# Kernel tuning notes

Measured on AMD Instinct MI355X. Metric: run time of the kernel, lower is better.

The kernel has to match this reference:

```python
import jax, jax.numpy as jnp
import numpy as np

DIM = 512
WIN = 7
HEADS = 16
N = WIN * WIN            # 49 tokens per window
NW = 64                  # windows per image (56/7)^2
BATCH = 32               # images
B_ = BATCH * NW          # 2048 window-batches
TABLE = (2 * WIN - 1) ** 2  # 169


def _relative_position_index(win):
    # Faithful to the TF construction in __init__.
    coords = np.stack(np.meshgrid(np.arange(win), np.arange(win), indexing='ij'))
    coords = coords.reshape(2, -1).T                      # [N, 2]
    rel = coords[:, None, :] - coords[None, :, :]          # [N, N, 2]
    rel = rel + (win - 1)
    idx = rel[..., 0] * (2 * win - 1) + rel[..., 1]        # [N, N]
    return jnp.asarray(idx, dtype=jnp.int32)


def setup_inputs() -> dict:
    key = jax.random.key(0)
    ks = jax.random.split(key, 7)
    x = jax.random.normal(ks[0], (B_, N, DIM), dtype=jnp.float32)
    # shifted-window additive mask: 0 where allowed, -100 where blocked
    mask = jnp.where(jax.random.uniform(ks[1], (NW, N, N)) < 0.8, 0.0, -100.0).astype(jnp.float32)
    qkv_w = jax.random.normal(ks[2], (DIM, 3 * DIM), dtype=jnp.float32) * 0.02
    qkv_b = jax.random.normal(ks[3], (3 * DIM,), dtype=jnp.float32) * 0.02
    proj_w = jax.random.normal(ks[4], (DIM, DIM), dtype=jnp.float32) * 0.02
    proj_b = jax.random.normal(ks[5], (DIM,), dtype=jnp.float32) * 0.02
    rel_table = jax.random.normal(ks[6], (TABLE, HEADS), dtype=jnp.float32) * 0.02
    rel_index = _relative_position_index(WIN)
    return {"x": x, "mask": mask, "qkv_w": qkv_w, "qkv_b": qkv_b,
            "proj_w": proj_w, "proj_b": proj_b,
            "rel_table": rel_table, "rel_index": rel_index}


def reference(x, mask, qkv_w, qkv_b, proj_w, proj_b, rel_table, rel_index):
    B, n, C = x.shape
    hd = C // HEADS
    scale = hd ** (-0.5)
    # qkv projection -> [3, B, H, N, hd]
    qkv = (x @ qkv_w + qkv_b).reshape(B, n, 3, HEADS, hd).transpose(2, 0, 3, 1, 4)
    q, k, v = qkv[0] * scale, qkv[1], qkv[2]
    attn = jnp.einsum('bhnd,bhmd->bhnm', q, k)             # [B, H, N, N]
    # relative position bias gather: [N*N] -> [N, N, H] -> [H, N, N]
    bias = rel_table[rel_index.reshape(-1)].reshape(n, n, HEADS).transpose(2, 0, 1)
    attn = attn + bias[None]
    nW = mask.shape[0]
    attn = attn.reshape(B // nW, nW, HEADS, n, n) + mask[None, :, None]
    attn = attn.reshape(-1, HEADS, n, n)
    attn = jax.nn.softmax(attn, axis=-1)
    out = jnp.einsum('bhnm,bhmd->bhnd', attn, v)           # [B, H, N, hd]
    out = out.transpose(0, 2, 1, 3).reshape(B, n, C)
    return out @ proj_w + proj_b
```

## Files before the change

### kernel.cpp

```cpp
#include <hip/hip_runtime.h>

typedef unsigned short ushort_t;
typedef short short8 __attribute__((ext_vector_type(8)));
typedef float f32x4 __attribute__((ext_vector_type(4)));
typedef unsigned short ushort4v __attribute__((ext_vector_type(4)));

__device__ __forceinline__ ushort_t f2bf(float f) {
    unsigned int u = __float_as_uint(f);
    u = (u + 0x7fffu + ((u >> 16) & 1u)) >> 16;
    return (ushort_t)u;
}

__device__ __forceinline__ void async16(void* lds, const void* g) {
    __builtin_amdgcn_global_load_lds(
        (const __attribute__((address_space(1))) unsigned int*)g,
        (__attribute__((address_space(3))) unsigned int*)lds, 16, 0, 0);
}

__global__ void conv_x_kernel(const float* __restrict__ in, ushort_t* __restrict__ out) {
    int i = blockIdx.x * 256 + threadIdx.x;
    float4 v = ((const float4*)in)[i];
    ushort4v o;
    o.x = f2bf(v.x); o.y = f2bf(v.y); o.z = f2bf(v.z); o.w = f2bf(v.w);
    ((ushort4v*)out)[i] = o;
}

__global__ void prep_weights(const float* __restrict__ qkv_w, const float* __restrict__ proj_w,
                             ushort_t* __restrict__ wtq, ushort_t* __restrict__ wtp) {
    int o = blockIdx.x * 256 + threadIdx.x;
    if (o < 1536 * 512) {
        int n = o >> 9, k = o & 511;
        wtq[o] = f2bf(qkv_w[k * 1536 + n]);
    }
    if (o < 512 * 512) {
        int n = o >> 9, k = o & 511;
        wtp[o] = f2bf(proj_w[k * 512 + n]);
    }
}

__global__ void build_cm(const float* __restrict__ mask, const float* __restrict__ rel_table,
                         const int* __restrict__ rel_index, float* __restrict__ cm) {
    int o = blockIdx.x * 256 + threadIdx.x;
    int c = o & 63, r = (o >> 6) & 63, h = (o >> 12) & 15, w = o >> 16;
    float v = -30000.0f;
    if (r < 49 && c < 49)
        v = rel_table[rel_index[r * 49 + c] * 16 + h] + mask[w * 2401 + r * 49 + c];
    cm[o] = v;
}


#define STAGE(ldsbase, gbase) do {                                              \
    _Pragma("unroll")                                                           \
    for (int j_ = 0; j_ < 2; ++j_) {                                            \
        const int idx_ = j_ * 512 + tid;                                        \
        const int row_ = idx_ >> 3;                                             \
        const int sc_  = (((idx_ & 7) ^ (row_ & 7)) << 3);                      \
        async16((char*)(ldsbase) + idx_ * 16, (gbase) + (size_t)row_ * K + sc_);\
    }                                                                           \
} while (0)

#define VM0 asm volatile("s_waitcnt vmcnt(0)" ::: "memory")

#define LOADA(buf, mh) do {                                                     \
    _Pragma("unroll")                                                           \
    for (int f_ = 0; f_ < 4; ++f_) {                                            \
        const int ar_ = wr + ((mh) * 4 + f_) * 16 + lr;                         \
        _Pragma("unroll")                                                       \
        for (int ks_ = 0; ks_ < 2; ++ks_)                                       \
            af[f_][ks_] = *(const short8*)&As[buf][ar_ * 64 + ((ks_ * 32 + lk * 8) ^ ((ar_ & 7) << 3))]; \
    }                                                                           \
} while (0)

#define LOADB(buf) do {                                                         \
    _Pragma("unroll")                                                           \
    for (int g_ = 0; g_ < 4; ++g_) {                                            \
        const int br_ = wc + g_ * 16 + lr;                                      \
        _Pragma("unroll")                                                       \
        for (int ks_ = 0; ks_ < 2; ++ks_)                                       \
            bf[g_][ks_] = *(const short8*)&Bs[buf][br_ * 64 + ((ks_ * 32 + lk * 8) ^ ((br_ & 7) << 3))]; \
    }                                                                           \
} while (0)

#define WAITLDS do {                                                            \
    __builtin_amdgcn_s_barrier();                                               \
    asm volatile("s_waitcnt lgkmcnt(0)" ::: "memory");                          \
    __builtin_amdgcn_sched_barrier(0);                                          \
} while (0)

#define MFMAH(mh) do {                                                          \
    __builtin_amdgcn_s_setprio(1);                                              \
    _Pragma("unroll")                                                           \
    for (int f_ = 0; f_ < 4; ++f_)                                              \
        _Pragma("unroll")                                                       \
        for (int g_ = 0; g_ < 4; ++g_)                                          \
            _Pragma("unroll")                                                   \
            for (int ks_ = 0; ks_ < 2; ++ks_)                                   \
                acc[(mh) * 4 + f_][g_] = __builtin_amdgcn_mfma_f32_16x16x32_bf16( \
                    bf[g_][ks_], af[f_][ks_], acc[(mh) * 4 + f_][g_], 0, 0, 0); \
    __builtin_amdgcn_s_setprio(0);                                              \
} while (0)

#define TILE(buf, DOSTAGE, koff) do {                                           \
    short8 af[4][2], bf[4][2];                                                  \
    LOADB(buf); LOADA(buf, 0);                                                  \
    if (DOSTAGE) {                                                              \
        STAGE(&As[(buf) ^ 1][0],    A  + a0 + (koff));                          \
        STAGE(&As[(buf) ^ 1][8192], A  + a1 + (koff));                          \
        STAGE(&Bs[(buf) ^ 1][0],    Bt + b0 + (koff));                          \
        STAGE(&Bs[(buf) ^ 1][8192], Bt + b1 + (koff));                          \
    }                                                                           \
    WAITLDS;                                                                    \
    MFMAH(0);                                                                   \
    LOADA(buf, 1);       \
    WAITLDS;                                                                    \
    MFMAH(1);                                                                   \
    VM0;                      \
    __builtin_amdgcn_s_barrier();                                               \
} while (0)

template<int NB_N, int NSTR, bool QKV, int K>
__global__ __launch_bounds__(512, 2)
void gemm8(const ushort_t* __restrict__ A, const ushort_t* __restrict__ Bt,
           const float* __restrict__ bias, void* __restrict__ out)
{
    __shared__ alignas(16) ushort_t As[2][256 * 64];
    __shared__ alignas(16) ushort_t Bs[2][256 * 64];

    const int tid = threadIdx.x;
    const int wid = tid >> 6, lane = tid & 63;
    const int lr = lane & 15, lk = lane >> 4;
    const int wr = (wid >> 2) * 128;
    const int wc = (wid & 3) * 64;

    const int chunk = gridDim.x >> 3;
    const int wg = ((int)blockIdx.x & 7) * chunk + ((int)blockIdx.x >> 3);
    const int nb = wg % NB_N;
    const int mb = wg / NB_N;
    const int m0 = mb << 8, n0 = nb << 8;

    const size_t a0 = (size_t)m0 * K;
    const size_t a1 = (size_t)(m0 + 128) * K;
    const size_t b0 = (size_t)n0 * K;
    const size_t b1 = (size_t)(n0 + 128) * K;

    f32x4 acc[8][4];
#pragma unroll
    for (int f = 0; f < 8; ++f)
#pragma unroll
        for (int g = 0; g < 4; ++g)
#pragma unroll
            for (int r = 0; r < 4; ++r) acc[f][g][r] = 0.f;

    STAGE(&As[0][0],    A  + a0);
    STAGE(&As[0][8192], A  + a1);
    STAGE(&Bs[0][0],    Bt + b0);
    STAGE(&Bs[0][8192], Bt + b1);
    VM0;
    __builtin_amdgcn_s_barrier();

    const int KT = K >> 6;
    for (int t = 0; t < KT; t += 2) {
        const int c1 = (t + 1) << 6;
        const int c2 = (t + 2) << 6;
        TILE(0, true,          c1);
        TILE(1, (t + 2 < KT),  c2);
    }

#pragma unroll
    for (int f = 0; f < 8; ++f) {
        const int row = m0 + wr + f * 16 + lr;
#pragma unroll
        for (int g = 0; g < 4; ++g) {
            const int col = n0 + wc + g * 16 + lk * 4;
            const float4 bv = *(const float4*)&bias[col];
            float v0 = acc[f][g][0] + bv.x;
            float v1 = acc[f][g][1] + bv.y;
            float v2 = acc[f][g][2] + bv.z;
            float v3 = acc[f][g][3] + bv.w;
            if (QKV) {
                if (col < 512) {
                    v0 *= 0.17677669529663689f; v1 *= 0.17677669529663689f;
                    v2 *= 0.17677669529663689f; v3 *= 0.17677669529663689f;
                }
                ushort4v o;
                o.x = f2bf(v0); o.y = f2bf(v1); o.z = f2bf(v2); o.w = f2bf(v3);
                *(ushort4v*)&((ushort_t*)out)[(size_t)row * NSTR + col] = o;
            } else {
                float4 o; o.x = v0; o.y = v1; o.z = v2; o.w = v3;
                *(float4*)&((float*)out)[(size_t)row * NSTR + col] = o;
            }
        }
    }
}

#define PL_STRIDE 80
#define VT_STRIDE 88
__global__ __launch_bounds__(256, 2)
void attn_kernel(const ushort_t* __restrict__ qkv, const float* __restrict__ cm,
                 ushort_t* __restrict__ out)
{
    __shared__ alignas(16) char smem[4 * 64 * PL_STRIDE * 2 + 4 * 32 * VT_STRIDE * 2];
    float* cmf = (float*)smem;
    ushort_t* Pl = (ushort_t*)smem;
    ushort_t* vT = (ushort_t*)(smem + 4 * 64 * PL_STRIDE * 2);

    const int w = blockIdx.x, h = blockIdx.y, ig = blockIdx.z;
    const int tid = threadIdx.x;
    const int wid = tid >> 6, lane = tid & 63;
    const int lr = lane & 15, lk = lane >> 4;
    const int b = (ig * 4 + wid) * 64 + w;

    const float* cmsrc = cm + ((size_t)(w * 16 + h) << 12);
    for (int t = tid; t < 4096; t += 256)
        cmf[(t >> 6) * 65 + (t & 63)] = cmsrc[t];
    __syncthreads();

    const size_t base = (size_t)b * 49 * 1536 + h * 32;

    short8 aq[4], bk[4];
#pragma unroll
    for (int i = 0; i < 4; ++i) {
        int n = i * 16 + lr; n = n > 48 ? 48 : n;
        aq[i] = *(const short8*)&qkv[base + (size_t)n * 1536 + lk * 8];
    }
#pragma unroll
    for (int j = 0; j < 4; ++j) {
        int m = j * 16 + lr; m = m > 48 ? 48 : m;
        bk[j] = *(const short8*)&qkv[base + 512 + (size_t)m * 1536 + lk * 8];
    }

    f32x4 s[4][4];
#pragma unroll
    for (int i = 0; i < 4; ++i)
#pragma unroll
        for (int j = 0; j < 4; ++j)
#pragma unroll
            for (int r = 0; r < 4; ++r) s[i][j][r] = 0.f;
#pragma unroll
    for (int i = 0; i < 4; ++i)
#pragma unroll
        for (int j = 0; j < 4; ++j)
            s[i][j] = __builtin_amdgcn_mfma_f32_16x16x32_bf16(aq[i], bk[j], s[i][j], 0, 0, 0);

    short8 vv[4];
#pragma unroll
    for (int t = 0; t < 4; ++t)
#pragma unroll
        for (int e = 0; e < 8; ++e) vv[t][e] = 0;
    if (lane < 49) {
        const ushort_t* vp = &qkv[base + 1024 + (size_t)lane * 1536];
#pragma unroll
        for (int t = 0; t < 4; ++t) vv[t] = *(const short8*)(vp + t * 8);
    }
    ushort_t* vTw = vT + wid * 32 * VT_STRIDE;
#pragma unroll
    for (int t = 0; t < 4; ++t)
#pragma unroll
        for (int e = 0; e < 8; ++e)
            vTw[(t * 8 + e) * VT_STRIDE + lane] = (ushort_t)vv[t][e];

#pragma unroll
    for (int i = 0; i < 4; ++i) {
#pragma unroll
        for (int r = 0; r < 4; ++r) {
            const int row = i * 16 + lk * 4 + r;
            float v0 = s[i][0][r] + cmf[row * 65 + lr];
            float v1 = s[i][1][r] + cmf[row * 65 + 16 + lr];
            float v2 = s[i][2][r] + cmf[row * 65 + 32 + lr];
            float v3 = s[i][3][r] + cmf[row * 65 + 48 + lr];
            float mx = fmaxf(fmaxf(v0, v1), fmaxf(v2, v3));
#pragma unroll
            for (int t = 1; t < 16; t <<= 1) mx = fmaxf(mx, __shfl_xor(mx, t, 64));
            v0 = __expf(v0 - mx); v1 = __expf(v1 - mx);
            v2 = __expf(v2 - mx); v3 = __expf(v3 - mx);
            float sm = v0 + v1 + v2 + v3;
#pragma unroll
            for (int t = 1; t < 16; t <<= 1) sm += __shfl_xor(sm, t, 64);
            const float inv = 1.0f / sm;
            s[i][0][r] = v0 * inv; s[i][1][r] = v1 * inv;
            s[i][2][r] = v2 * inv; s[i][3][r] = v3 * inv;
        }
    }
    __syncthreads();

    ushort_t* Pw = Pl + wid * 64 * PL_STRIDE;
#pragma unroll
    for (int i = 0; i < 4; ++i)
#pragma unroll
        for (int j = 0; j < 4; ++j)
#pragma unroll
            for (int r = 0; r < 4; ++r)
                Pw[(i * 16 + lk * 4 + r) * PL_STRIDE + j * 16 + lr] = f2bf(s[i][j][r]);

    f32x4 o[4][2];
#pragma unroll
    for (int i = 0; i < 4; ++i)
#pragma unroll
        for (int jb = 0; jb < 2; ++jb)
#pragma unroll
            for (int r = 0; r < 4; ++r) o[i][jb][r] = 0.f;
#pragma unroll
    for (int ks = 0; ks < 2; ++ks) {
        short8 pa[4], vb[2];
#pragma unroll
        for (int i = 0; i < 4; ++i)
            pa[i] = *(const short8*)&Pw[(i * 16 + lr) * PL_STRIDE + ks * 32 + lk * 8];
#pragma unroll
        for (int jb = 0; jb < 2; ++jb)
            vb[jb] = *(const short8*)&vTw[(jb * 16 + lr) * VT_STRIDE + ks * 32 + lk * 8];
#pragma unroll
        for (int i = 0; i < 4; ++i)
#pragma unroll
            for (int jb = 0; jb < 2; ++jb)
                o[i][jb] = __builtin_amdgcn_mfma_f32_16x16x32_bf16(vb[jb], pa[i], o[i][jb], 0, 0, 0);
    }

    const size_t obase = (size_t)b * 49 * 512 + h * 32;
#pragma unroll
    for (int i = 0; i < 4; ++i) {
        const int n = i * 16 + lr;
        if (n < 49) {
#pragma unroll
            for (int jb = 0; jb < 2; ++jb) {
                ushort4v ov;
                ov.x = f2bf(o[i][jb][0]); ov.y = f2bf(o[i][jb][1]);
                ov.z = f2bf(o[i][jb][2]); ov.w = f2bf(o[i][jb][3]);
                *(ushort4v*)&out[obase + (size_t)n * 512 + jb * 16 + lk * 4] = ov;
            }
        }
    }
}

extern "C" void kernel_launch(void* const* d_in, const int* in_sizes, int n_in,
                              void* d_out, int out_size, void* d_ws, size_t ws_size,
                              hipStream_t stream)
{
    const float* x         = (const float*)d_in[0];
    const float* mask      = (const float*)d_in[1];
    const float* qkv_w     = (const float*)d_in[2];
    const float* qkv_b     = (const float*)d_in[3];
    const float* proj_w    = (const float*)d_in[4];
    const float* proj_b    = (const float*)d_in[5];
    const float* rel_table = (const float*)d_in[6];
    const int*   rel_index = (const int*)d_in[7];

    char* ws = (char*)d_ws;
    ushort_t* xb  = (ushort_t*)ws;
    ushort_t* qkv = (ushort_t*)(ws + 102760448);
    ushort_t* wtq = (ushort_t*)(ws + 411041792);
    ushort_t* wtp = (ushort_t*)(ws + 412614656);
    float*    cm  = (float*)  (ws + 413138944);

    conv_x_kernel<<<50176, 256, 0, stream>>>(x, xb);
    prep_weights<<<3072, 256, 0, stream>>>(qkv_w, proj_w, wtq, wtp);
    build_cm<<<16384, 256, 0, stream>>>(mask, rel_table, rel_index, cm);

    gemm8<6, 1536, true, 512><<<2352, 512, 0, stream>>>(xb, wtq, qkv_b, qkv);

    attn_kernel<<<dim3(64, 16, 8), 256, 0, stream>>>(qkv, cm, xb);

    gemm8<2, 512, false, 512><<<784, 512, 0, stream>>>(xb, wtp, proj_b, d_out);
}
```

Before: 643.9 us.

## Deepen GEMM prefetch to two tiles in flight with partial vmcnt waits

Reworks the bf16 GEMM main loop so two K-tiles are prefetched before the loop and each tile waits only with vmcnt(8), letting the next tile's global-to-LDS loads stay in flight while the current tile computes. The refill of a buffer is issued after the compute on it finishes and a barrier, instead of staging into the other buffer and waiting for all loads at the end of every tile. The aim is to hide global memory latency better. It adds a second barrier per tile and depends on the vmcnt count matching exactly eight outstanding async loads per stage.

New measurement: 633.8 us. Within noise of the previous version (-1.6%).

```diff
diff --git a/kernel.cpp b/kernel.cpp
--- a/kernel.cpp
+++ b/kernel.cpp
@@ -59,6 +59,7 @@
     }                                                                           \
 } while (0)
 
+#define VM8 asm volatile("s_waitcnt vmcnt(8)" ::: "memory")
 #define VM0 asm volatile("s_waitcnt vmcnt(0)" ::: "memory")
 
 #define LOADA(buf, mh) do {                                                     \
@@ -81,8 +82,7 @@
     }                                                                           \
 } while (0)
 
-#define WAITLDS do {                                                            \
-    __builtin_amdgcn_s_barrier();                                               \
+#define LGKM0 do {                                                              \
     asm volatile("s_waitcnt lgkmcnt(0)" ::: "memory");                          \
     __builtin_amdgcn_sched_barrier(0);                                          \
 } while (0)
@@ -100,22 +100,23 @@
     __builtin_amdgcn_s_setprio(0);                                              \
 } while (0)
 
-#define TILE(buf, DOSTAGE, koff) do {                                           \
+#define TILE(buf, VMWAIT, DOSTAGE, koff) do {                                   \
+    VMWAIT;                                                                     \
+    __builtin_amdgcn_s_barrier();        \
     short8 af[4][2], bf[4][2];                                                  \
     LOADB(buf); LOADA(buf, 0);                                                  \
+    LGKM0;                                                                      \
+    MFMAH(0);                                                                   \
+    LOADA(buf, 1);                                                              \
+    LGKM0;                                                                      \
+    MFMAH(1);                                                                   \
+    __builtin_amdgcn_s_barrier();               \
     if (DOSTAGE) {                                                              \
-        STAGE(&As[(buf) ^ 1][0],    A  + a0 + (koff));                          \
-        STAGE(&As[(buf) ^ 1][8192], A  + a1 + (koff));                          \
-        STAGE(&Bs[(buf) ^ 1][0],    Bt + b0 + (koff));                          \
-        STAGE(&Bs[(buf) ^ 1][8192], Bt + b1 + (koff));                          \
+        STAGE(&As[buf][0],    A  + a0 + (koff));                                \
+        STAGE(&As[buf][8192], A  + a1 + (koff));                                \
+        STAGE(&Bs[buf][0],    Bt + b0 + (koff));                                \
+        STAGE(&Bs[buf][8192], Bt + b1 + (koff));                                \
     }                                                                           \
-    WAITLDS;                                                                    \
-    MFMAH(0);                                                                   \
-    LOADA(buf, 1);       \
-    WAITLDS;                                                                    \
-    MFMAH(1);                                                                   \
-    VM0;                      \
-    __builtin_amdgcn_s_barrier();                                               \
 } while (0)
 
 template<int NB_N, int NSTR, bool QKV, int K>
@@ -155,16 +156,18 @@
     STAGE(&As[0][8192], A  + a1);
     STAGE(&Bs[0][0],    Bt + b0);
     STAGE(&Bs[0][8192], Bt + b1);
-    VM0;
-    __builtin_amdgcn_s_barrier();
+    STAGE(&As[1][0],    A  + a0 + 64);
+    STAGE(&As[1][8192], A  + a1 + 64);
+    STAGE(&Bs[1][0],    Bt + b0 + 64);
+    STAGE(&Bs[1][8192], Bt + b1 + 64);
 
     const int KT = K >> 6;
-    for (int t = 0; t < KT; t += 2) {
-        const int c1 = (t + 1) << 6;
-        const int c2 = (t + 2) << 6;
-        TILE(0, true,          c1);
-        TILE(1, (t + 2 < KT),  c2);
-    }
+    for (int t = 0; t < KT - 2; t += 2) {
+        TILE(0, VM8, true, (t + 2) << 6);
+        TILE(1, VM8, true, (t + 3) << 6);
+    }
+    TILE(0, VM8, false, 0);
+    TILE(1, VM0, false, 0);
 
 #pragma unroll
     for (int f = 0; f < 8; ++f) {
```
